# Kernel optimization log

Measured on AMD Instinct MI355X. Metric: run time of the kernel, lower is better.

The kernel has to match this reference:

```python
import jax, jax.numpy as jnp
import numpy as np

N = 100000
E = 1600000
F_IN = 128
HID = 128
C = 10
NEG_SLOPE = 0.2


def setup_inputs() -> dict:
    key = jax.random.key(0)
    ks = jax.random.split(key, 12)
    x = jax.random.normal(ks[0], (N, F_IN), dtype=jnp.float32)
    edge_index = jax.random.randint(ks[1], (2, E), 0, N, dtype=jnp.int64)
    batch = jnp.zeros((N,), dtype=jnp.int64)
    s1 = 1.0 / np.sqrt(F_IN)
    s2 = 1.0 / np.sqrt(HID)
    return {
        "x": x,
        "edge_index": edge_index,
        "batch": batch,
        "W1": jax.random.normal(ks[2], (F_IN, HID), dtype=jnp.float32) * s1,
        "a_src1": jax.random.normal(ks[3], (HID,), dtype=jnp.float32) * s2,
        "a_dst1": jax.random.normal(ks[4], (HID,), dtype=jnp.float32) * s2,
        "b1": jnp.zeros((HID,), dtype=jnp.float32),
        "W2": jax.random.normal(ks[5], (HID, HID), dtype=jnp.float32) * s2,
        "a_src2": jax.random.normal(ks[6], (HID,), dtype=jnp.float32) * s2,
        "a_dst2": jax.random.normal(ks[7], (HID,), dtype=jnp.float32) * s2,
        "b2": jnp.zeros((HID,), dtype=jnp.float32),
        "Wlin": jax.random.normal(ks[8], (HID, C), dtype=jnp.float32) * s2,
        "blin": jnp.zeros((C,), dtype=jnp.float32),
    }


def gat_conv(x, src, dst, W, a_src, a_dst, b):
    # PyG GATConv, heads=1: h = xW; alpha_e = softmax_dst(leaky_relu(a_src.h[src] + a_dst.h[dst]))
    h = x @ W                                  # [N, H]
    alpha_s = h @ a_src                        # [N]
    alpha_d = h @ a_dst                        # [N]
    e = jax.nn.leaky_relu(alpha_s[src] + alpha_d[dst], NEG_SLOPE)  # [E]
    m = jax.ops.segment_max(e, dst, num_segments=N)                # per-dst max (stable softmax)
    ex = jnp.exp(e - m[dst])
    denom = jax.ops.segment_sum(ex, dst, num_segments=N)
    alpha = ex / (denom[dst] + 1e-16)          # [E]
    out = jax.ops.segment_sum(h[src] * alpha[:, None], dst, num_segments=N)
    return out + b


def reference(x, edge_index, batch, W1, a_src1, a_dst1, b1, W2, a_src2, a_dst2, b2, Wlin, blin):
    x = x.astype(jnp.float32)
    loops = jnp.arange(N, dtype=edge_index.dtype)
    src = jnp.concatenate([edge_index[0], loops])  # add_self_loops=True
    dst = jnp.concatenate([edge_index[1], loops])
    h = jax.nn.relu(gat_conv(x, src, dst, W1, a_src1, a_dst1, b1))
    h = jax.nn.relu(gat_conv(h, src, dst, W2, a_src2, a_dst2, b2))
    # dropout(p=0.5) is identity in eval mode
    return h @ Wlin + blin
```

## Files before the change

kernel.cpp:

```cpp
#include <hip/hip_runtime.h>

#define N_NODES 100000
#define N_EDGES 1600000
#define TOTE    (N_EDGES + N_NODES)
#define NEG     0.2f
#define NB      ((N_NODES + 255) >> 8)
#define BCAP    5120

typedef __attribute__((ext_vector_type(8))) short bf16x8;
typedef __attribute__((ext_vector_type(4))) float floatx4;

__device__ __forceinline__ unsigned short f2bf(float f) {
  unsigned int u = __float_as_uint(f);
  u += 0x7fffu + ((u >> 16) & 1u);
  return (unsigned short)(u >> 16);
}
__device__ __forceinline__ float bf_lo(unsigned int r) { return __uint_as_float(r << 16); }
__device__ __forceinline__ float bf_hi(unsigned int r) { return __uint_as_float(r & 0xffff0000u); }

__global__ __launch_bounds__(256) void k_wprep(const float* __restrict__ W1, const float* __restrict__ W2,
                                               unsigned short* __restrict__ B1hi, unsigned short* __restrict__ B1lo,
                                               unsigned short* __restrict__ B2hi, unsigned short* __restrict__ B2lo,
                                               int* __restrict__ bucketCnt) {
  int b = blockIdx.x;
  int t = threadIdx.x;
  if (b == 16) {
    for (int i = t; i < NB * 16; i += 256) bucketCnt[i] = 0;
    return;
  }
  const float* W = (b < 8) ? W1 : W2;
  unsigned short* Bh = (b < 8) ? B1hi : B2hi;
  unsigned short* Bl = (b < 8) ? B1lo : B2lo;
  int ntile = b & 7;
  int kq = t >> 6, lane = t & 63;
  int q = lane >> 4, m = lane & 15;
  int n = ntile * 16 + m;
  union { unsigned short us[8]; uint4 u4; } hi, lo;
#pragma unroll
  for (int j = 0; j < 8; ++j) {
    int k = kq * 32 + q * 8 + j;
    float w = W[(size_t)k * 128 + n];
    unsigned int u = __float_as_uint(w);
    hi.us[j] = (unsigned short)(u >> 16);
    float res = w - __uint_as_float(u & 0xffff0000u);
    lo.us[j] = f2bf(res);
  }
  size_t fo = ((size_t)(ntile * 4 + kq) * 64 + lane) * 8;
  *reinterpret_cast<uint4*>(Bh + fo) = hi.u4;
  *reinterpret_cast<uint4*>(Bl + fo) = lo.u4;
}

__global__ __launch_bounds__(256) void k_binA(const int* __restrict__ ei, int* __restrict__ bucketCnt,
                                              unsigned int* __restrict__ binned) {
  __shared__ int hist[NB];
  __shared__ int cur[NB];
  int t = threadIdx.x;
  for (int b = t; b < NB; b += 256) hist[b] = 0;
  __syncthreads();
  unsigned int pk[16]; int bk[16];
#pragma unroll
  for (int j = 0; j < 16; ++j) {
    int idx = blockIdx.x * 4096 + j * 256 + t;
    if (idx < N_EDGES) {
      int s = ei[idx], d = ei[N_EDGES + idx];
      bk[j] = d >> 8;
      pk[j] = ((unsigned int)s << 8) | (unsigned int)(d & 255);
      atomicAdd(&hist[bk[j]], 1);
    } else bk[j] = -1;
  }
  __syncthreads();
  for (int b = t; b < NB; b += 256) {
    int h = hist[b];
    if (h) cur[b] = b * BCAP + atomicAdd(&bucketCnt[b * 16], h);
  }
  __syncthreads();
#pragma unroll
  for (int j = 0; j < 16; ++j) {
    if (bk[j] >= 0) {
      int pos = atomicAdd(&cur[bk[j]], 1);
      binned[pos] = pk[j];
    }
  }
}

__global__ __launch_bounds__(512) void k_bin_scan(const int* __restrict__ bucketCnt,
                                                  int* __restrict__ binOffs) {
  __shared__ int sc[512];
  int t = threadIdx.x;
  int v = (t < NB) ? bucketCnt[t * 16] : 0;
  sc[t] = v; __syncthreads();
  for (int off = 1; off < 512; off <<= 1) {
    int x = (t >= off) ? sc[t - off] : 0;
    __syncthreads();
    sc[t] += x;
    __syncthreads();
  }
  int excl = sc[t] - v;
  if (t <= NB) binOffs[t] = excl;
}

__global__ __launch_bounds__(256) void k_binB(const unsigned int* __restrict__ binned,
                                              const int* __restrict__ binOffs,
                                              int* __restrict__ offs, int* __restrict__ srcs) {
  __shared__ int cnt[256];
  __shared__ int sc[256];
  __shared__ int cur[256];
  int b = blockIdx.x;
  int t = threadIdx.x;
  int node0 = b << 8;
  int nNodes = min(256, N_NODES - node0);
  int cntE = binOffs[b + 1] - binOffs[b];
  int e0 = b * BCAP, e1 = e0 + cntE;
  int base = binOffs[b] + node0;

  cnt[t] = 0; __syncthreads();
  for (int i = e0 + t; i < e1; i += 256) atomicAdd(&cnt[binned[i] & 255u], 1);
  __syncthreads();

  int v = (t < nNodes) ? cnt[t] + 1 : 0;
  sc[t] = v; __syncthreads();
  for (int off = 1; off < 256; off <<= 1) {
    int x = (t >= off) ? sc[t - off] : 0;
    __syncthreads();
    sc[t] += x;
    __syncthreads();
  }
  int excl = sc[t] - v;
  if (t < nNodes) {
    offs[node0 + t] = base + excl;
    srcs[base + excl] = node0 + t;
  }
  cur[t] = excl + 1;
  __syncthreads();

  for (int i = e0 + t; i < e1; i += 256) {
    unsigned int e = binned[i];
    int j = (int)(e & 255u);
    int s = (int)(e >> 8);
    int p = atomicAdd(&cur[j], 1);
    srcs[base + p] = s;
  }
  if (b == 0 && t == 0) offs[N_NODES] = TOTE;
}

template <bool SPLIT>
__global__ __launch_bounds__(256) void k_gemm_mfma(const void* __restrict__ Aptr,
                                                   const unsigned short* __restrict__ Bhi,
                                                   const unsigned short* __restrict__ Blo,
                                                   unsigned short* __restrict__ Cb,
                                                   const float* __restrict__ avS, const float* __restrict__ avD,
                                                   float* __restrict__ aS, float* __restrict__ aD,
                                                   float* __restrict__ slotS, float* __restrict__ slotD) {
  __shared__ unsigned short sC[64 * 136];
  __shared__ float redS[64 * 4], redD[64 * 4];
  __shared__ float mS[64], mD[64];
  int t = threadIdx.x;
  int w = t >> 6, lane = t & 63;
  int q = lane >> 4, m = lane & 15;
  int rbase = blockIdx.x * 64;

  floatx4 acc[4][2];
#pragma unroll
  for (int mt = 0; mt < 4; ++mt)
#pragma unroll
    for (int nt = 0; nt < 2; ++nt) acc[mt][nt] = (floatx4){0.f, 0.f, 0.f, 0.f};

#pragma unroll
  for (int k0 = 0; k0 < 4; ++k0) {
    bf16x8 Bh[2], Bl[2], Ah[4], Al[4];
#pragma unroll
    for (int nt = 0; nt < 2; ++nt) {
      int ntg = w * 2 + nt;
      size_t fo = ((size_t)(ntg * 4 + k0) * 64 + lane) * 8;
      Bh[nt] = *reinterpret_cast<const bf16x8*>(Bhi + fo);
      Bl[nt] = *reinterpret_cast<const bf16x8*>(Blo + fo);
    }
#pragma unroll
    for (int mt = 0; mt < 4; ++mt) {
      int row = rbase + mt * 16 + m;
      row = min(row, N_NODES - 1);
      if constexpr (SPLIT) {
        const float* ap = (const float*)Aptr + (size_t)row * 128 + k0 * 32 + q * 8;
        float4 v0 = *reinterpret_cast<const float4*>(ap);
        float4 v1 = *reinterpret_cast<const float4*>(ap + 4);
        float av[8] = {v0.x, v0.y, v0.z, v0.w, v1.x, v1.y, v1.z, v1.w};
        union { unsigned short us[8]; bf16x8 v; } uh, ul;
#pragma unroll
        for (int j = 0; j < 8; ++j) {
          unsigned int u = __float_as_uint(av[j]);
          uh.us[j] = (unsigned short)(u >> 16);
          float res = av[j] - __uint_as_float(u & 0xffff0000u);
          ul.us[j] = f2bf(res);
        }
        Ah[mt] = uh.v; Al[mt] = ul.v;
      } else {
        const unsigned short* ap = (const unsigned short*)Aptr + (size_t)row * 128 + k0 * 32 + q * 8;
        Ah[mt] = *reinterpret_cast<const bf16x8*>(ap);
      }
    }
#pragma unroll
    for (int mt = 0; mt < 4; ++mt)
#pragma unroll
      for (int nt = 0; nt < 2; ++nt) {
        acc[mt][nt] = __builtin_amdgcn_mfma_f32_16x16x32_bf16(Ah[mt], Bh[nt], acc[mt][nt], 0, 0, 0);
        acc[mt][nt] = __builtin_amdgcn_mfma_f32_16x16x32_bf16(Ah[mt], Bl[nt], acc[mt][nt], 0, 0, 0);
        if constexpr (SPLIT)
          acc[mt][nt] = __builtin_amdgcn_mfma_f32_16x16x32_bf16(Al[mt], Bh[nt], acc[mt][nt], 0, 0, 0);
      }
  }

  float avs[2], avd[2];
#pragma unroll
  for (int nt = 0; nt < 2; ++nt) {
    int c = w * 32 + nt * 16 + m;
    avs[nt] = avS[c];
    avd[nt] = avD[c];
  }
#pragma unroll
  for (int mt = 0; mt < 4; ++mt)
#pragma unroll
    for (int r = 0; r < 4; ++r) {
      float ps = acc[mt][0][r] * avs[0] + acc[mt][1][r] * avs[1];
      float pd = acc[mt][0][r] * avd[0] + acc[mt][1][r] * avd[1];
      ps += __shfl_xor(ps, 1); pd += __shfl_xor(pd, 1);
      ps += __shfl_xor(ps, 2); pd += __shfl_xor(pd, 2);
      ps += __shfl_xor(ps, 4); pd += __shfl_xor(pd, 4);
      ps += __shfl_xor(ps, 8); pd += __shfl_xor(pd, 8);
      if (m == 0) {
        int rl = mt * 16 + q * 4 + r;
        redS[rl * 4 + w] = ps;
        redD[rl * 4 + w] = pd;
      }
    }

#pragma unroll
  for (int mt = 0; mt < 4; ++mt)
#pragma unroll
    for (int nt = 0; nt < 2; ++nt)
#pragma unroll
      for (int r = 0; r < 4; ++r) {
        int rl = mt * 16 + q * 4 + r;
        int cl = w * 32 + nt * 16 + m;
        sC[rl * 136 + cl] = f2bf(acc[mt][nt][r]);
      }
  __syncthreads();

#pragma unroll
  for (int i = 0; i < 4; ++i) {
    int idx = i * 256 + t;
    int rl = idx >> 4, kk = idx & 15;
    int gr = rbase + rl;
    if (gr < N_NODES)
      *reinterpret_cast<uint4*>(Cb + (size_t)gr * 128 + kk * 8) =
          *reinterpret_cast<const uint4*>(sC + rl * 136 + kk * 8);
  }

  if (t < 64) {
    int gr = rbase + t;
    bool ok = gr < N_NODES;
    float ps = redS[t * 4] + redS[t * 4 + 1] + redS[t * 4 + 2] + redS[t * 4 + 3];
    float pd = redD[t * 4] + redD[t * 4 + 1] + redD[t * 4 + 2] + redD[t * 4 + 3];
    if (ok) { aS[gr] = ps; aD[gr] = pd; }
    mS[t] = ok ? ps : -1e30f;
    mD[t] = ok ? pd : -1e30f;
  }
  __syncthreads();
#pragma unroll
  for (int off = 32; off > 0; off >>= 1) {
    if (t < off) { mS[t] = fmaxf(mS[t], mS[t + off]); mD[t] = fmaxf(mD[t], mD[t + off]); }
    __syncthreads();
  }
  if (t == 0) { slotS[blockIdx.x] = mS[0]; slotD[blockIdx.x] = mD[0]; }
}

__global__ __launch_bounds__(256) void k_gmax(const float* __restrict__ slotS,
                                              const float* __restrict__ slotD,
                                              int n, float* __restrict__ gMh) {
  __shared__ float sS[256], sD[256];
  int t = threadIdx.x;
  float ms = -1e30f, md = -1e30f;
  for (int i = t; i < n; i += 256) { ms = fmaxf(ms, slotS[i]); md = fmaxf(md, slotD[i]); }
  sS[t] = ms; sD[t] = md;
  __syncthreads();
#pragma unroll
  for (int off = 128; off > 0; off >>= 1) {
    if (t < off) { sS[t] = fmaxf(sS[t], sS[t + off]); sD[t] = fmaxf(sD[t], sD[t + off]); }
    __syncthreads();
  }
  if (t == 0) {
    float M = sS[0] + sD[0];
    gMh[0] = (M > 0.f) ? M : NEG * M;
  }
}

#define FMA8(E, R)                                     \
  do {                                                 \
    acc[0] += (E) * bf_lo((R).x); acc[1] += (E) * bf_hi((R).x); \
    acc[2] += (E) * bf_lo((R).y); acc[3] += (E) * bf_hi((R).y); \
    acc[4] += (E) * bf_lo((R).z); acc[5] += (E) * bf_hi((R).z); \
    acc[6] += (E) * bf_lo((R).w); acc[7] += (E) * bf_hi((R).w); \
  } while (0)

#define LDG(R0, R1, R2, R3, E0, E1, E2, E3, J)                                                   \
  do {                                                                                           \
    float2 q0 = pairs[pbase + (J) + 0];                                                          \
    float2 q1 = pairs[pbase + (J) + 1];                                                          \
    float2 q2 = pairs[pbase + (J) + 2];                                                          \
    float2 q3 = pairs[pbase + (J) + 3];                                                          \
    E0 = q0.x; E1 = q1.x; E2 = q2.x; E3 = q3.x;                                                  \
    R0 = *reinterpret_cast<const uint4*>(hbl + ((size_t)(unsigned)__float_as_int(q0.y) << 7));   \
    R1 = *reinterpret_cast<const uint4*>(hbl + ((size_t)(unsigned)__float_as_int(q1.y) << 7));   \
    R2 = *reinterpret_cast<const uint4*>(hbl + ((size_t)(unsigned)__float_as_int(q2.y) << 7));   \
    R3 = *reinterpret_cast<const uint4*>(hbl + ((size_t)(unsigned)__float_as_int(q3.y) << 7));   \
  } while (0)
#define FMAG(R0, R1, R2, R3, E0, E1, E2, E3) \
  do { FMA8(E0, R0); FMA8(E1, R1); FMA8(E2, R2); FMA8(E3, R3); } while (0)

template <bool FINAL>
__global__ __launch_bounds__(256) void k_aggregate(const unsigned short* __restrict__ hb,
                                                   const float* __restrict__ aS,
                                                   const float* __restrict__ aD,
                                                   const int* __restrict__ offs,
                                                   const int* __restrict__ srcs,
                                                   const float* __restrict__ bias,
                                                   const float* __restrict__ gMh,
                                                   unsigned short* __restrict__ outb,
                                                   const float* __restrict__ Wl,
                                                   const float* __restrict__ bl,
                                                   float* __restrict__ out) {
  __shared__ float2 pairs[16 * 17];
  __shared__ float sWt[FINAL ? 10 * 144 : 1];
  __shared__ float sbl[FINAL ? 16 : 1];
  int t = threadIdx.x;
  if constexpr (FINAL) {
    if (t < 128) {
      int jj = t >> 5, ii = t & 31;
#pragma unroll
      for (int c = 0; c < 10; ++c) sWt[c * 144 + jj * 36 + ii] = Wl[t * 10 + c];
    }
    if (t < 10) sbl[t] = bl[t];
    __syncthreads();
  }
  int g = t >> 4;
  int l = t & 15;
  int dst = blockIdx.x * 16 + g;
  float Mh = gMh[0];
  int beg = offs[dst], end = offs[dst + 1];
  float adn = aD[dst];
  float denom = 0.f;
  float acc[8];
#pragma unroll
  for (int k = 0; k < 8; ++k) acc[k] = 0.f;
  const int pbase = g * 17;
  const unsigned short* hbl = hb + l * 8;

  uint4 ra0, ra1, ra2, ra3, rb0, rb1, rb2, rb3;
  float ea0, ea1, ea2, ea3, eb0, eb1, eb2, eb3;

  for (int chunk = beg; chunk < end; chunk += 16) {
    int i = chunk + l;
    float ex = 0.f; int s = 0;
    if (i < end) {
      s = srcs[i];
      float e = aS[s] + adn;
      e = (e > 0.f) ? e : NEG * e;
      ex = __expf(e - Mh);
    }
    denom += ex;
    pairs[pbase + l] = make_float2(ex, __int_as_float(s));
    int cnt = end - chunk; if (cnt > 16) cnt = 16;
    LDG(ra0, ra1, ra2, ra3, ea0, ea1, ea2, ea3, 0);
    int j = 0;
    for (;;) {
      bool more = (j + 4) < cnt;
      if (more) LDG(rb0, rb1, rb2, rb3, eb0, eb1, eb2, eb3, j + 4);
      FMAG(ra0, ra1, ra2, ra3, ea0, ea1, ea2, ea3);
      j += 4;
      if (!more) break;
      bool more2 = (j + 4) < cnt;
      if (more2) LDG(ra0, ra1, ra2, ra3, ea0, ea1, ea2, ea3, j + 4);
      FMAG(rb0, rb1, rb2, rb3, eb0, eb1, eb2, eb3);
      j += 4;
      if (!more2) break;
    }
  }

  denom += __shfl_xor(denom, 1);
  denom += __shfl_xor(denom, 2);
  denom += __shfl_xor(denom, 4);
  denom += __shfl_xor(denom, 8);
  float inv = 1.f / (denom + 1e-16f);
  float4 b0 = *reinterpret_cast<const float4*>(bias + l * 8);
  float4 b1 = *reinterpret_cast<const float4*>(bias + l * 8 + 4);
  float o0 = fmaxf(acc[0] * inv + b0.x, 0.f), o1 = fmaxf(acc[1] * inv + b0.y, 0.f);
  float o2 = fmaxf(acc[2] * inv + b0.z, 0.f), o3 = fmaxf(acc[3] * inv + b0.w, 0.f);
  float o4 = fmaxf(acc[4] * inv + b1.x, 0.f), o5 = fmaxf(acc[5] * inv + b1.y, 0.f);
  float o6 = fmaxf(acc[6] * inv + b1.z, 0.f), o7 = fmaxf(acc[7] * inv + b1.w, 0.f);

  if constexpr (!FINAL) {
    union { unsigned short us[8]; uint4 u4; } oo;
    oo.us[0] = f2bf(o0); oo.us[1] = f2bf(o1); oo.us[2] = f2bf(o2); oo.us[3] = f2bf(o3);
    oo.us[4] = f2bf(o4); oo.us[5] = f2bf(o5); oo.us[6] = f2bf(o6); oo.us[7] = f2bf(o7);
    *reinterpret_cast<uint4*>(outb + (size_t)dst * 128 + l * 8) = oo.u4;
  } else {
    float p[10];
#pragma unroll
    for (int c = 0; c < 10; ++c) {
      const float4* wp = reinterpret_cast<const float4*>(&sWt[c * 144 + (l >> 2) * 36 + (l & 3) * 8]);
      float4 w0 = wp[0], w1 = wp[1];
      p[c] = o0 * w0.x + o1 * w0.y + o2 * w0.z + o3 * w0.w +
             o4 * w1.x + o5 * w1.y + o6 * w1.z + o7 * w1.w;
    }
#pragma unroll
    for (int c = 0; c < 10; ++c) {
      p[c] += __shfl_xor(p[c], 1);
      p[c] += __shfl_xor(p[c], 2);
      p[c] += __shfl_xor(p[c], 4);
      p[c] += __shfl_xor(p[c], 8);
    }
    if (l == 0) {
      float* orow = out + (size_t)dst * 10;
      *reinterpret_cast<float2*>(orow + 0) = make_float2(p[0] + sbl[0], p[1] + sbl[1]);
      *reinterpret_cast<float2*>(orow + 2) = make_float2(p[2] + sbl[2], p[3] + sbl[3]);
      *reinterpret_cast<float2*>(orow + 4) = make_float2(p[4] + sbl[4], p[5] + sbl[5]);
      *reinterpret_cast<float2*>(orow + 6) = make_float2(p[6] + sbl[6], p[7] + sbl[7]);
      *reinterpret_cast<float2*>(orow + 8) = make_float2(p[8] + sbl[8], p[9] + sbl[9]);
    }
  }
}

extern "C" void kernel_launch(void* const* d_in, const int* in_sizes, int n_in,
                              void* d_out, int out_size, void* d_ws, size_t ws_size,
                              hipStream_t stream) {
  const float* x   = (const float*)d_in[0];
  const int*   ei  = (const int*)d_in[1];
  const float* W1  = (const float*)d_in[3];
  const float* as1 = (const float*)d_in[4];
  const float* ad1 = (const float*)d_in[5];
  const float* b1  = (const float*)d_in[6];
  const float* W2  = (const float*)d_in[7];
  const float* as2 = (const float*)d_in[8];
  const float* ad2 = (const float*)d_in[9];
  const float* b2  = (const float*)d_in[10];
  const float* Wl  = (const float*)d_in[11];
  const float* bl  = (const float*)d_in[12];
  float* out = (float*)d_out;

  char* p = (char*)d_ws;
  unsigned short* hb   = (unsigned short*)p; p += (size_t)N_NODES * 128 * sizeof(unsigned short);
  unsigned short* hagg = (unsigned short*)p; p += (size_t)N_NODES * 128 * sizeof(unsigned short);
  float* aS    = (float*)p; p += (size_t)N_NODES * sizeof(float);
  float* aD    = (float*)p; p += (size_t)N_NODES * sizeof(float);
  int* offs    = (int*)p;   p += (size_t)(N_NODES + 4) * sizeof(int);
  int* srcs    = (int*)p;   p += (size_t)TOTE * sizeof(int);
  int* bucketCnt = (int*)p; p += (size_t)NB * 16 * sizeof(int);
  int* binOffs   = (int*)p; p += (size_t)(NB + 4) * sizeof(int);
  float* slotS = (float*)p; p += 2048 * sizeof(float);
  float* slotD = (float*)p; p += 2048 * sizeof(float);
  float* gMh = (float*)p;   p += 4 * sizeof(float);
  unsigned short* B1hi = (unsigned short*)p; p += 128 * 128 * sizeof(unsigned short);
  unsigned short* B1lo = (unsigned short*)p; p += 128 * 128 * sizeof(unsigned short);
  unsigned short* B2hi = (unsigned short*)p; p += 128 * 128 * sizeof(unsigned short);
  unsigned short* B2lo = (unsigned short*)p; p += 128 * 128 * sizeof(unsigned short);
  unsigned int* binned = (unsigned int*)hagg;

  int binBlocks = (N_EDGES + 4095) / 4096;

  k_wprep<<<17, 256, 0, stream>>>(W1, W2, B1hi, B1lo, B2hi, B2lo, bucketCnt);
  k_binA<<<binBlocks, 256, 0, stream>>>(ei, bucketCnt, binned);
  k_bin_scan<<<1, 512, 0, stream>>>(bucketCnt, binOffs);
  k_binB<<<NB, 256, 0, stream>>>(binned, binOffs, offs, srcs);

  int gemmBlocks = (N_NODES + 63) / 64;
  int aggBlocks  = N_NODES / 16;

  k_gemm_mfma<true><<<gemmBlocks, 256, 0, stream>>>(x, B1hi, B1lo, hb, as1, ad1, aS, aD, slotS, slotD);
  k_gmax<<<1, 256, 0, stream>>>(slotS, slotD, gemmBlocks, gMh);
  k_aggregate<false><<<aggBlocks, 256, 0, stream>>>(hb, aS, aD, offs, srcs, b1, gMh, hagg,
                                                    nullptr, nullptr, nullptr);
  k_gemm_mfma<false><<<gemmBlocks, 256, 0, stream>>>(hagg, B2hi, B2lo, hb, as2, ad2, aS, aD, slotS, slotD);
  k_gmax<<<1, 256, 0, stream>>>(slotS, slotD, gemmBlocks, gMh);
  k_aggregate<true><<<aggBlocks, 256, 0, stream>>>(hb, aS, aD, offs, srcs, b2, gMh, hagg,
                                                   Wl, bl, out);
}
```

Baseline: 353.1 us.

## Precompute per-edge softmax weights and denominators in separate edge-prep kernel

Edge attention weights (exp of leaky-relu scores) and per-destination denominators are moved out of the aggregation kernel into a new edge-prep kernel that writes (weight, src) pairs to a global array. The CSR source list now packs the local destination index into its low bits so edge-prep can work per 256-node bucket with shared-memory atomics. The aggregation kernel then streams the precomputed pairs straight from global memory, with no shared-memory staging or shuffle reduction, and prefetches them one group ahead. This adds an extra kernel launch and about 13.6 MB of pair traffic per layer in exchange for a simpler, more latency-tolerant gather loop.

Result: slower. 397.5 us (+12.6%).

```diff
diff --git a/kernel.cpp b/kernel.cpp
--- a/kernel.cpp
+++ b/kernel.cpp
@@ -101,7 +101,7 @@
 
 __global__ __launch_bounds__(256) void k_binB(const unsigned int* __restrict__ binned,
                                               const int* __restrict__ binOffs,
-                                              int* __restrict__ offs, int* __restrict__ srcs) {
+                                              int* __restrict__ offs, unsigned int* __restrict__ srcs) {
   __shared__ int cnt[256];
   __shared__ int sc[256];
   __shared__ int cur[256];
@@ -128,7 +128,7 @@
   int excl = sc[t] - v;
   if (t < nNodes) {
     offs[node0 + t] = base + excl;
-    srcs[base + excl] = node0 + t;
+    srcs[base + excl] = ((unsigned int)(node0 + t) << 8) | (unsigned int)t;
   }
   cur[t] = excl + 1;
   __syncthreads();
@@ -136,9 +136,8 @@
   for (int i = e0 + t; i < e1; i += 256) {
     unsigned int e = binned[i];
     int j = (int)(e & 255u);
-    int s = (int)(e >> 8);
     int p = atomicAdd(&cur[j], 1);
-    srcs[base + p] = s;
+    srcs[base + p] = e;
   }
   if (b == 0 && t == 0) offs[N_NODES] = TOTE;
 }
@@ -293,6 +292,37 @@
   }
 }
 
+__global__ __launch_bounds__(256) void k_edgeprep(const unsigned int* __restrict__ srcs,
+                                                  const int* __restrict__ binOffs,
+                                                  const float* __restrict__ aS,
+                                                  const float* __restrict__ aD,
+                                                  const float* __restrict__ gMh,
+                                                  float2* __restrict__ pairEx,
+                                                  float* __restrict__ denomG) {
+  __shared__ float sden[256];
+  int b = blockIdx.x;
+  int t = threadIdx.x;
+  int node0 = b << 8;
+  int nNodes = min(256, N_NODES - node0);
+  int e0 = binOffs[b] + node0;
+  int e1 = binOffs[b + 1] + node0 + nNodes;
+  float Mh = gMh[0];
+  sden[t] = 0.f;
+  __syncthreads();
+  for (int i = e0 + t; i < e1; i += 256) {
+    unsigned int pk = srcs[i];
+    int j = (int)(pk & 255u);
+    int s = (int)(pk >> 8);
+    float e = aS[s] + aD[node0 + j];
+    e = (e > 0.f) ? e : NEG * e;
+    float ex = __expf(e - Mh);
+    pairEx[i] = make_float2(ex, __int_as_float(s));
+    atomicAdd(&sden[j], ex);
+  }
+  __syncthreads();
+  if (t < nNodes) denomG[node0 + t] = sden[t];
+}
+
 #define FMA8(E, R)                                     \
   do {                                                 \
     acc[0] += (E) * bf_lo((R).x); acc[1] += (E) * bf_hi((R).x); \
@@ -301,34 +331,35 @@
     acc[6] += (E) * bf_lo((R).w); acc[7] += (E) * bf_hi((R).w); \
   } while (0)
 
-#define LDG(R0, R1, R2, R3, E0, E1, E2, E3, J)                                                   \
-  do {                                                                                           \
-    float2 q0 = pairs[pbase + (J) + 0];                                                          \
-    float2 q1 = pairs[pbase + (J) + 1];                                                          \
-    float2 q2 = pairs[pbase + (J) + 2];                                                          \
-    float2 q3 = pairs[pbase + (J) + 3];                                                          \
-    E0 = q0.x; E1 = q1.x; E2 = q2.x; E3 = q3.x;                                                  \
-    R0 = *reinterpret_cast<const uint4*>(hbl + ((size_t)(unsigned)__float_as_int(q0.y) << 7));   \
-    R1 = *reinterpret_cast<const uint4*>(hbl + ((size_t)(unsigned)__float_as_int(q1.y) << 7));   \
-    R2 = *reinterpret_cast<const uint4*>(hbl + ((size_t)(unsigned)__float_as_int(q2.y) << 7));   \
-    R3 = *reinterpret_cast<const uint4*>(hbl + ((size_t)(unsigned)__float_as_int(q3.y) << 7));   \
+#define LOADP(Q0, Q1, Q2, Q3, J)                               \
+  do {                                                         \
+    Q0 = ((J) + 0 < n) ? pp[(J) + 0] : zf2;                    \
+    Q1 = ((J) + 1 < n) ? pp[(J) + 1] : zf2;                    \
+    Q2 = ((J) + 2 < n) ? pp[(J) + 2] : zf2;                    \
+    Q3 = ((J) + 3 < n) ? pp[(J) + 3] : zf2;                    \
   } while (0)
-#define FMAG(R0, R1, R2, R3, E0, E1, E2, E3) \
-  do { FMA8(E0, R0); FMA8(E1, R1); FMA8(E2, R2); FMA8(E3, R3); } while (0)
+
+#define GATH(R0, R1, R2, R3, Q0, Q1, Q2, Q3)                                                       \
+  do {                                                                                             \
+    R0 = *reinterpret_cast<const uint4*>(hbl + ((size_t)(unsigned)__float_as_int((Q0).y) << 7));   \
+    R1 = *reinterpret_cast<const uint4*>(hbl + ((size_t)(unsigned)__float_as_int((Q1).y) << 7));   \
+    R2 = *reinterpret_cast<const uint4*>(hbl + ((size_t)(unsigned)__float_as_int((Q2).y) << 7));   \
+    R3 = *reinterpret_cast<const uint4*>(hbl + ((size_t)(unsigned)__float_as_int((Q3).y) << 7));   \
+  } while (0)
+
+#define FMAG(R0, R1, R2, R3, Q0, Q1, Q2, Q3) \
+  do { FMA8((Q0).x, R0); FMA8((Q1).x, R1); FMA8((Q2).x, R2); FMA8((Q3).x, R3); } while (0)
 
 template <bool FINAL>
 __global__ __launch_bounds__(256) void k_aggregate(const unsigned short* __restrict__ hb,
-                                                   const float* __restrict__ aS,
-                                                   const float* __restrict__ aD,
+                                                   const float2* __restrict__ pairEx,
                                                    const int* __restrict__ offs,
-                                                   const int* __restrict__ srcs,
+                                                   const float* __restrict__ denomG,
                                                    const float* __restrict__ bias,
-                                                   const float* __restrict__ gMh,
                                                    unsigned short* __restrict__ outb,
                                                    const float* __restrict__ Wl,
                                                    const float* __restrict__ bl,
                                                    float* __restrict__ out) {
-  __shared__ float2 pairs[16 * 17];
   __shared__ float sWt[FINAL ? 10 * 144 : 1];
   __shared__ float sbl[FINAL ? 16 : 1];
   int t = threadIdx.x;
@@ -344,52 +375,39 @@
   int g = t >> 4;
   int l = t & 15;
   int dst = blockIdx.x * 16 + g;
-  float Mh = gMh[0];
   int beg = offs[dst], end = offs[dst + 1];
-  float adn = aD[dst];
-  float denom = 0.f;
+  int n = end - beg;
+  float den = denomG[dst];
   float acc[8];
 #pragma unroll
   for (int k = 0; k < 8; ++k) acc[k] = 0.f;
-  const int pbase = g * 17;
+  const float2* pp = pairEx + beg;
   const unsigned short* hbl = hb + l * 8;
-
+  const float2 zf2 = make_float2(0.f, 0.f);
+
+  float2 qa0, qa1, qa2, qa3, qb0, qb1, qb2, qb3;
   uint4 ra0, ra1, ra2, ra3, rb0, rb1, rb2, rb3;
-  float ea0, ea1, ea2, ea3, eb0, eb1, eb2, eb3;
-
-  for (int chunk = beg; chunk < end; chunk += 16) {
-    int i = chunk + l;
-    float ex = 0.f; int s = 0;
-    if (i < end) {
-      s = srcs[i];
-      float e = aS[s] + adn;
-      e = (e > 0.f) ? e : NEG * e;
-      ex = __expf(e - Mh);
-    }
-    denom += ex;
-    pairs[pbase + l] = make_float2(ex, __int_as_float(s));
-    int cnt = end - chunk; if (cnt > 16) cnt = 16;
-    LDG(ra0, ra1, ra2, ra3, ea0, ea1, ea2, ea3, 0);
-    int j = 0;
-    for (;;) {
-      bool more = (j + 4) < cnt;
-      if (more) LDG(rb0, rb1, rb2, rb3, eb0, eb1, eb2, eb3, j + 4);
-      FMAG(ra0, ra1, ra2, ra3, ea0, ea1, ea2, ea3);
-      j += 4;
-      if (!more) break;
-      bool more2 = (j + 4) < cnt;
-      if (more2) LDG(ra0, ra1, ra2, ra3, ea0, ea1, ea2, ea3, j + 4);
-      FMAG(rb0, rb1, rb2, rb3, eb0, eb1, eb2, eb3);
-      j += 4;
-      if (!more2) break;
-    }
-  }
-
-  denom += __shfl_xor(denom, 1);
-  denom += __shfl_xor(denom, 2);
-  denom += __shfl_xor(denom, 4);
-  denom += __shfl_xor(denom, 8);
-  float inv = 1.f / (denom + 1e-16f);
+
+  LOADP(qa0, qa1, qa2, qa3, 0);
+  if (4 < n) LOADP(qb0, qb1, qb2, qb3, 4);
+  GATH(ra0, ra1, ra2, ra3, qa0, qa1, qa2, qa3);
+  int j = 0;
+  for (;;) {
+    bool m1 = (j + 4) < n;
+    if (m1) GATH(rb0, rb1, rb2, rb3, qb0, qb1, qb2, qb3);
+    FMAG(ra0, ra1, ra2, ra3, qa0, qa1, qa2, qa3);
+    if ((j + 8) < n) LOADP(qa0, qa1, qa2, qa3, j + 8);
+    j += 4;
+    if (!m1) break;
+    bool m2 = (j + 4) < n;
+    if (m2) GATH(ra0, ra1, ra2, ra3, qa0, qa1, qa2, qa3);
+    FMAG(rb0, rb1, rb2, rb3, qb0, qb1, qb2, qb3);
+    if ((j + 8) < n) LOADP(qb0, qb1, qb2, qb3, j + 8);
+    j += 4;
+    if (!m2) break;
+  }
+
+  float inv = 1.f / (den + 1e-16f);
   float4 b0 = *reinterpret_cast<const float4*>(bias + l * 8);
   float4 b1 = *reinterpret_cast<const float4*>(bias + l * 8 + 4);
   float o0 = fmaxf(acc[0] * inv + b0.x, 0.f), o1 = fmaxf(acc[1] * inv + b0.y, 0.f);
@@ -452,7 +470,7 @@
   float* aS    = (float*)p; p += (size_t)N_NODES * sizeof(float);
   float* aD    = (float*)p; p += (size_t)N_NODES * sizeof(float);
   int* offs    = (int*)p;   p += (size_t)(N_NODES + 4) * sizeof(int);
-  int* srcs    = (int*)p;   p += (size_t)TOTE * sizeof(int);
+  unsigned int* srcs = (unsigned int*)p; p += (size_t)TOTE * sizeof(unsigned int);
   int* bucketCnt = (int*)p; p += (size_t)NB * 16 * sizeof(int);
   int* binOffs   = (int*)p; p += (size_t)(NB + 4) * sizeof(int);
   float* slotS = (float*)p; p += 2048 * sizeof(float);
@@ -462,6 +480,8 @@
   unsigned short* B1lo = (unsigned short*)p; p += 128 * 128 * sizeof(unsigned short);
   unsigned short* B2hi = (unsigned short*)p; p += 128 * 128 * sizeof(unsigned short);
   unsigned short* B2lo = (unsigned short*)p; p += 128 * 128 * sizeof(unsigned short);
+  float* denomG = (float*)p; p += (size_t)N_NODES * sizeof(float);
+  float2* pairEx = (float2*)p; p += (size_t)TOTE * sizeof(float2);
   unsigned int* binned = (unsigned int*)hagg;
 
   int binBlocks = (N_EDGES + 4095) / 4096;
@@ -476,10 +496,12 @@
 
   k_gemm_mfma<true><<<gemmBlocks, 256, 0, stream>>>(x, B1hi, B1lo, hb, as1, ad1, aS, aD, slotS, slotD);
   k_gmax<<<1, 256, 0, stream>>>(slotS, slotD, gemmBlocks, gMh);
-  k_aggregate<false><<<aggBlocks, 256, 0, stream>>>(hb, aS, aD, offs, srcs, b1, gMh, hagg,
+  k_edgeprep<<<NB, 256, 0, stream>>>(srcs, binOffs, aS, aD, gMh, pairEx, denomG);
+  k_aggregate<false><<<aggBlocks, 256, 0, stream>>>(hb, pairEx, offs, denomG, b1, hagg,
                                                     nullptr, nullptr, nullptr);
   k_gemm_mfma<false><<<gemmBlocks, 256, 0, stream>>>(hagg, B2hi, B2lo, hb, as2, ad2, aS, aD, slotS, slotD);
   k_gmax<<<1, 256, 0, stream>>>(slotS, slotD, gemmBlocks, gMh);
-  k_aggregate<true><<<aggBlocks, 256, 0, stream>>>(hb, aS, aD, offs, srcs, b2, gMh, hagg,
+  k_edgeprep<<<NB, 256, 0, stream>>>(srcs, binOffs, aS, aD, gMh, pairEx, denomG);
+  k_aggregate<true><<<aggBlocks, 256, 0, stream>>>(hb, pairEx, offs, denomG, b2, hagg,
                                                    Wl, bl, out);
 }
```

## Remove scan and gmax kernels via atomics, shrink aggregate blocks, simplify gather loop

Applied to the files above, without the earlier changes.

Three small kernels are removed. The bucket prefix scan is folded into each binB block as a redundant block-level reduction over preceding buckets. The per-block max slots plus the separate k_gmax kernel are replaced by an order-preserving float encoding with global atomicMax, zeroed in k_wprep. The aggregate kernel moves from 256 to 128 threads per block (8 destinations per block), and its double-buffered software-pipelined gather is replaced by a plain unrolled loop of four loads with a scalar tail. This saves launch and serialization overhead, but binB now does O(NB) redundant reads per block and the gather may expose more load latency.

Result: slower. 403.8 us (+14.4%).

```diff
diff --git a/kernel.cpp b/kernel.cpp
--- a/kernel.cpp
+++ b/kernel.cpp
@@ -18,14 +18,24 @@
 __device__ __forceinline__ float bf_lo(unsigned int r) { return __uint_as_float(r << 16); }
 __device__ __forceinline__ float bf_hi(unsigned int r) { return __uint_as_float(r & 0xffff0000u); }
 
+__device__ __forceinline__ unsigned int fenc(float f) {
+  unsigned int u = __float_as_uint(f);
+  return (u & 0x80000000u) ? ~u : (u | 0x80000000u);
+}
+__device__ __forceinline__ float fdec(unsigned int c) {
+  unsigned int u = (c & 0x80000000u) ? (c & 0x7fffffffu) : ~c;
+  return __uint_as_float(u);
+}
+
 __global__ __launch_bounds__(256) void k_wprep(const float* __restrict__ W1, const float* __restrict__ W2,
                                                unsigned short* __restrict__ B1hi, unsigned short* __restrict__ B1lo,
                                                unsigned short* __restrict__ B2hi, unsigned short* __restrict__ B2lo,
-                                               int* __restrict__ bucketCnt) {
+                                               int* __restrict__ bucketCnt, unsigned int* __restrict__ gmx) {
   int b = blockIdx.x;
   int t = threadIdx.x;
   if (b == 16) {
     for (int i = t; i < NB * 16; i += 256) bucketCnt[i] = 0;
+    if (t < 4) gmx[t] = 0u;
     return;
   }
   const float* W = (b < 8) ? W1 : W2;
@@ -83,25 +93,10 @@
   }
 }
 
-__global__ __launch_bounds__(512) void k_bin_scan(const int* __restrict__ bucketCnt,
-                                                  int* __restrict__ binOffs) {
-  __shared__ int sc[512];
-  int t = threadIdx.x;
-  int v = (t < NB) ? bucketCnt[t * 16] : 0;
-  sc[t] = v; __syncthreads();
-  for (int off = 1; off < 512; off <<= 1) {
-    int x = (t >= off) ? sc[t - off] : 0;
-    __syncthreads();
-    sc[t] += x;
-    __syncthreads();
-  }
-  int excl = sc[t] - v;
-  if (t <= NB) binOffs[t] = excl;
-}
-
 __global__ __launch_bounds__(256) void k_binB(const unsigned int* __restrict__ binned,
-                                              const int* __restrict__ binOffs,
+                                              const int* __restrict__ bucketCnt,
                                               int* __restrict__ offs, int* __restrict__ srcs) {
+  __shared__ int red[256];
   __shared__ int cnt[256];
   __shared__ int sc[256];
   __shared__ int cur[256];
@@ -109,9 +104,19 @@
   int t = threadIdx.x;
   int node0 = b << 8;
   int nNodes = min(256, N_NODES - node0);
-  int cntE = binOffs[b + 1] - binOffs[b];
+
+  int a = 0;
+  for (int i = t; i < b; i += 256) a += bucketCnt[i * 16];
+  red[t] = a; __syncthreads();
+#pragma unroll
+  for (int off = 128; off > 0; off >>= 1) {
+    if (t < off) red[t] += red[t + off];
+    __syncthreads();
+  }
+  int pre = red[0];
+  int cntE = bucketCnt[b * 16];
   int e0 = b * BCAP, e1 = e0 + cntE;
-  int base = binOffs[b] + node0;
+  int base = pre + node0;
 
   cnt[t] = 0; __syncthreads();
   for (int i = e0 + t; i < e1; i += 256) atomicAdd(&cnt[binned[i] & 255u], 1);
@@ -150,7 +155,7 @@
                                                    unsigned short* __restrict__ Cb,
                                                    const float* __restrict__ avS, const float* __restrict__ avD,
                                                    float* __restrict__ aS, float* __restrict__ aD,
-                                                   float* __restrict__ slotS, float* __restrict__ slotD) {
+                                                   unsigned int* __restrict__ gmx) {
   __shared__ unsigned short sC[64 * 136];
   __shared__ float redS[64 * 4], redD[64 * 4];
   __shared__ float mS[64], mD[64];
@@ -270,26 +275,9 @@
     if (t < off) { mS[t] = fmaxf(mS[t], mS[t + off]); mD[t] = fmaxf(mD[t], mD[t + off]); }
     __syncthreads();
   }
-  if (t == 0) { slotS[blockIdx.x] = mS[0]; slotD[blockIdx.x] = mD[0]; }
-}
-
-__global__ __launch_bounds__(256) void k_gmax(const float* __restrict__ slotS,
-                                              const float* __restrict__ slotD,
-                                              int n, float* __restrict__ gMh) {
-  __shared__ float sS[256], sD[256];
-  int t = threadIdx.x;
-  float ms = -1e30f, md = -1e30f;
-  for (int i = t; i < n; i += 256) { ms = fmaxf(ms, slotS[i]); md = fmaxf(md, slotD[i]); }
-  sS[t] = ms; sD[t] = md;
-  __syncthreads();
-#pragma unroll
-  for (int off = 128; off > 0; off >>= 1) {
-    if (t < off) { sS[t] = fmaxf(sS[t], sS[t + off]); sD[t] = fmaxf(sD[t], sD[t + off]); }
-    __syncthreads();
-  }
   if (t == 0) {
-    float M = sS[0] + sD[0];
-    gMh[0] = (M > 0.f) ? M : NEG * M;
+    atomicMax(&gmx[0], fenc(mS[0]));
+    atomicMax(&gmx[1], fenc(mD[0]));
   }
 }
 
@@ -301,39 +289,24 @@
     acc[6] += (E) * bf_lo((R).w); acc[7] += (E) * bf_hi((R).w); \
   } while (0)
 
-#define LDG(R0, R1, R2, R3, E0, E1, E2, E3, J)                                                   \
-  do {                                                                                           \
-    float2 q0 = pairs[pbase + (J) + 0];                                                          \
-    float2 q1 = pairs[pbase + (J) + 1];                                                          \
-    float2 q2 = pairs[pbase + (J) + 2];                                                          \
-    float2 q3 = pairs[pbase + (J) + 3];                                                          \
-    E0 = q0.x; E1 = q1.x; E2 = q2.x; E3 = q3.x;                                                  \
-    R0 = *reinterpret_cast<const uint4*>(hbl + ((size_t)(unsigned)__float_as_int(q0.y) << 7));   \
-    R1 = *reinterpret_cast<const uint4*>(hbl + ((size_t)(unsigned)__float_as_int(q1.y) << 7));   \
-    R2 = *reinterpret_cast<const uint4*>(hbl + ((size_t)(unsigned)__float_as_int(q2.y) << 7));   \
-    R3 = *reinterpret_cast<const uint4*>(hbl + ((size_t)(unsigned)__float_as_int(q3.y) << 7));   \
-  } while (0)
-#define FMAG(R0, R1, R2, R3, E0, E1, E2, E3) \
-  do { FMA8(E0, R0); FMA8(E1, R1); FMA8(E2, R2); FMA8(E3, R3); } while (0)
-
 template <bool FINAL>
-__global__ __launch_bounds__(256) void k_aggregate(const unsigned short* __restrict__ hb,
+__global__ __launch_bounds__(128) void k_aggregate(const unsigned short* __restrict__ hb,
                                                    const float* __restrict__ aS,
                                                    const float* __restrict__ aD,
                                                    const int* __restrict__ offs,
                                                    const int* __restrict__ srcs,
                                                    const float* __restrict__ bias,
-                                                   const float* __restrict__ gMh,
+                                                   const unsigned int* __restrict__ gmx,
                                                    unsigned short* __restrict__ outb,
                                                    const float* __restrict__ Wl,
                                                    const float* __restrict__ bl,
                                                    float* __restrict__ out) {
-  __shared__ float2 pairs[16 * 17];
+  __shared__ float2 pairs[8 * 17];
   __shared__ float sWt[FINAL ? 10 * 144 : 1];
   __shared__ float sbl[FINAL ? 16 : 1];
   int t = threadIdx.x;
   if constexpr (FINAL) {
-    if (t < 128) {
+    {
       int jj = t >> 5, ii = t & 31;
 #pragma unroll
       for (int c = 0; c < 10; ++c) sWt[c * 144 + jj * 36 + ii] = Wl[t * 10 + c];
@@ -343,8 +316,9 @@
   }
   int g = t >> 4;
   int l = t & 15;
-  int dst = blockIdx.x * 16 + g;
-  float Mh = gMh[0];
+  int dst = blockIdx.x * 8 + g;
+  float M = fdec(gmx[0]) + fdec(gmx[1]);
+  float Mh = (M > 0.f) ? M : NEG * M;
   int beg = offs[dst], end = offs[dst + 1];
   float adn = aD[dst];
   float denom = 0.f;
@@ -352,10 +326,6 @@
 #pragma unroll
   for (int k = 0; k < 8; ++k) acc[k] = 0.f;
   const int pbase = g * 17;
-  const unsigned short* hbl = hb + l * 8;
-
-  uint4 ra0, ra1, ra2, ra3, rb0, rb1, rb2, rb3;
-  float ea0, ea1, ea2, ea3, eb0, eb1, eb2, eb3;
 
   for (int chunk = beg; chunk < end; chunk += 16) {
     int i = chunk + l;
@@ -368,23 +338,28 @@
     }
     denom += ex;
     pairs[pbase + l] = make_float2(ex, __int_as_float(s));
-    int cnt = end - chunk; if (cnt > 16) cnt = 16;
-    LDG(ra0, ra1, ra2, ra3, ea0, ea1, ea2, ea3, 0);
+    int cnt = min(16, end - chunk);
     int j = 0;
-    for (;;) {
-      bool more = (j + 4) < cnt;
-      if (more) LDG(rb0, rb1, rb2, rb3, eb0, eb1, eb2, eb3, j + 4);
-      FMAG(ra0, ra1, ra2, ra3, ea0, ea1, ea2, ea3);
-      j += 4;
-      if (!more) break;
-      bool more2 = (j + 4) < cnt;
-      if (more2) LDG(ra0, ra1, ra2, ra3, ea0, ea1, ea2, ea3, j + 4);
-      FMAG(rb0, rb1, rb2, rb3, eb0, eb1, eb2, eb3);
-      j += 4;
-      if (!more2) break;
-    }
-  }
-
+    for (; j + 4 <= cnt; j += 4) {
+      float2 p0 = pairs[pbase + j + 0];
+      float2 p1 = pairs[pbase + j + 1];
+      float2 p2 = pairs[pbase + j + 2];
+      float2 p3 = pairs[pbase + j + 3];
+      uint4 r0 = *reinterpret_cast<const uint4*>(hb + (size_t)__float_as_int(p0.y) * 128 + l * 8);
+      uint4 r1 = *reinterpret_cast<const uint4*>(hb + (size_t)__float_as_int(p1.y) * 128 + l * 8);
+      uint4 r2 = *reinterpret_cast<const uint4*>(hb + (size_t)__float_as_int(p2.y) * 128 + l * 8);
+      uint4 r3 = *reinterpret_cast<const uint4*>(hb + (size_t)__float_as_int(p3.y) * 128 + l * 8);
+      FMA8(p0.x, r0);
+      FMA8(p1.x, r1);
+      FMA8(p2.x, r2);
+      FMA8(p3.x, r3);
+    }
+    for (; j < cnt; ++j) {
+      float2 pp = pairs[pbase + j];
+      uint4 r = *reinterpret_cast<const uint4*>(hb + (size_t)__float_as_int(pp.y) * 128 + l * 8);
+      FMA8(pp.x, r);
+    }
+  }
   denom += __shfl_xor(denom, 1);
   denom += __shfl_xor(denom, 2);
   denom += __shfl_xor(denom, 4);
@@ -454,10 +429,7 @@
   int* offs    = (int*)p;   p += (size_t)(N_NODES + 4) * sizeof(int);
   int* srcs    = (int*)p;   p += (size_t)TOTE * sizeof(int);
   int* bucketCnt = (int*)p; p += (size_t)NB * 16 * sizeof(int);
-  int* binOffs   = (int*)p; p += (size_t)(NB + 4) * sizeof(int);
-  float* slotS = (float*)p; p += 2048 * sizeof(float);
-  float* slotD = (float*)p; p += 2048 * sizeof(float);
-  float* gMh = (float*)p;   p += 4 * sizeof(float);
+  unsigned int* gmx = (unsigned int*)p; p += 16 * sizeof(unsigned int);
   unsigned short* B1hi = (unsigned short*)p; p += 128 * 128 * sizeof(unsigned short);
   unsigned short* B1lo = (unsigned short*)p; p += 128 * 128 * sizeof(unsigned short);
   unsigned short* B2hi = (unsigned short*)p; p += 128 * 128 * sizeof(unsigned short);
@@ -466,20 +438,17 @@
 
   int binBlocks = (N_EDGES + 4095) / 4096;
 
-  k_wprep<<<17, 256, 0, stream>>>(W1, W2, B1hi, B1lo, B2hi, B2lo, bucketCnt);
+  k_wprep<<<17, 256, 0, stream>>>(W1, W2, B1hi, B1lo, B2hi, B2lo, bucketCnt, gmx);
   k_binA<<<binBlocks, 256, 0, stream>>>(ei, bucketCnt, binned);
-  k_bin_scan<<<1, 512, 0, stream>>>(bucketCnt, binOffs);
-  k_binB<<<NB, 256, 0, stream>>>(binned, binOffs, offs, srcs);
+  k_binB<<<NB, 256, 0, stream>>>(binned, bucketCnt, offs, srcs);
 
   int gemmBlocks = (N_NODES + 63) / 64;
-  int aggBlocks  = N_NODES / 16;
-
-  k_gemm_mfma<true><<<gemmBlocks, 256, 0, stream>>>(x, B1hi, B1lo, hb, as1, ad1, aS, aD, slotS, slotD);
-  k_gmax<<<1, 256, 0, stream>>>(slotS, slotD, gemmBlocks, gMh);
-  k_aggregate<false><<<aggBlocks, 256, 0, stream>>>(hb, aS, aD, offs, srcs, b1, gMh, hagg,
+  int aggBlocks  = N_NODES / 8;
+
+  k_gemm_mfma<true><<<gemmBlocks, 256, 0, stream>>>(x, B1hi, B1lo, hb, as1, ad1, aS, aD, gmx);
+  k_aggregate<false><<<aggBlocks, 128, 0, stream>>>(hb, aS, aD, offs, srcs, b1, gmx, hagg,
                                                     nullptr, nullptr, nullptr);
-  k_gemm_mfma<false><<<gemmBlocks, 256, 0, stream>>>(hagg, B2hi, B2lo, hb, as2, ad2, aS, aD, slotS, slotD);
-  k_gmax<<<1, 256, 0, stream>>>(slotS, slotD, gemmBlocks, gMh);
-  k_aggregate<true><<<aggBlocks, 256, 0, stream>>>(hb, aS, aD, offs, srcs, b2, gMh, hagg,
+  k_gemm_mfma<false><<<gemmBlocks, 256, 0, stream>>>(hagg, B2hi, B2lo, hb, as2, ad2, aS, aD, gmx + 2);
+  k_aggregate<true><<<aggBlocks, 128, 0, stream>>>(hb, aS, aD, offs, srcs, b2, gmx + 2, hagg,
                                                    Wl, bl, out);
 }
```

## Stage GEMM A tiles into LDS via async global_load_lds; simplify aggregate loop

Applied to the files above, without the earlier changes.

The GEMM kernel now loads its 64-row A tile into a padded LDS buffer with global_load_lds direct-to-LDS transfers before the MFMA loop, reads A fragments from LDS, and reuses that buffer for the output staging. This replaces strided per-lane global reads with coalesced bulk loads, and adds an occupancy hint of 4 blocks per CU. The aggregate kernel drops the manual double-buffered software prefetch in favour of a simple unroll-by-4 loop with a scalar tail, handing load scheduling to the compiler. The simpler loop may hide gather latency less well, and the larger LDS buffer (about 33KB in the split case) may limit occupancy.

New measurement: 347.6 us. About the same (-1.6%).

```diff
diff --git a/kernel.cpp b/kernel.cpp
--- a/kernel.cpp
+++ b/kernel.cpp
@@ -144,26 +144,44 @@
 }
 
 template <bool SPLIT>
-__global__ __launch_bounds__(256) void k_gemm_mfma(const void* __restrict__ Aptr,
+__global__ __launch_bounds__(256, 4) void k_gemm_mfma(const void* __restrict__ Aptr,
                                                    const unsigned short* __restrict__ Bhi,
                                                    const unsigned short* __restrict__ Blo,
                                                    unsigned short* __restrict__ Cb,
                                                    const float* __restrict__ avS, const float* __restrict__ avD,
                                                    float* __restrict__ aS, float* __restrict__ aD,
                                                    float* __restrict__ slotS, float* __restrict__ slotD) {
-  __shared__ unsigned short sC[64 * 136];
+  constexpr int SRCB  = SPLIT ? 512 : 256;
+  constexpr int ROWB  = SPLIT ? 528 : 272;
+  constexpr int ABYTES = 64 * ROWB;
+  constexpr int CHUNKS = ABYTES / 1024;
+  __shared__ char sbuf[ABYTES];
   __shared__ float redS[64 * 4], redD[64 * 4];
   __shared__ float mS[64], mD[64];
   int t = threadIdx.x;
   int w = t >> 6, lane = t & 63;
   int q = lane >> 4, m = lane & 15;
   int rbase = blockIdx.x * 64;
+  const char* Ab = (const char*)Aptr;
+
+  for (int c = w; c < CHUNKS; c += 4) {
+    int L = c * 1024 + lane * 16;
+    int r = L / ROWB;
+    int off = L - r * ROWB;
+    int gr = min(rbase + r, N_NODES - 1);
+    const char* src = (off < SRCB) ? (Ab + (size_t)gr * SRCB + off) : Ab;
+    __builtin_amdgcn_global_load_lds((const __attribute__((address_space(1))) void*)src,
+                                     (__attribute__((address_space(3))) void*)(sbuf + c * 1024),
+                                     16, 0, 0);
+  }
 
   floatx4 acc[4][2];
 #pragma unroll
   for (int mt = 0; mt < 4; ++mt)
 #pragma unroll
     for (int nt = 0; nt < 2; ++nt) acc[mt][nt] = (floatx4){0.f, 0.f, 0.f, 0.f};
+
+  __syncthreads();
 
 #pragma unroll
   for (int k0 = 0; k0 < 4; ++k0) {
@@ -177,12 +195,11 @@
     }
 #pragma unroll
     for (int mt = 0; mt < 4; ++mt) {
-      int row = rbase + mt * 16 + m;
-      row = min(row, N_NODES - 1);
+      int R = mt * 16 + m;
       if constexpr (SPLIT) {
-        const float* ap = (const float*)Aptr + (size_t)row * 128 + k0 * 32 + q * 8;
+        const char* ap = sbuf + R * ROWB + k0 * 128 + q * 32;
         float4 v0 = *reinterpret_cast<const float4*>(ap);
-        float4 v1 = *reinterpret_cast<const float4*>(ap + 4);
+        float4 v1 = *reinterpret_cast<const float4*>(ap + 16);
         float av[8] = {v0.x, v0.y, v0.z, v0.w, v1.x, v1.y, v1.z, v1.w};
         union { unsigned short us[8]; bf16x8 v; } uh, ul;
 #pragma unroll
@@ -194,8 +211,7 @@
         }
         Ah[mt] = uh.v; Al[mt] = ul.v;
       } else {
-        const unsigned short* ap = (const unsigned short*)Aptr + (size_t)row * 128 + k0 * 32 + q * 8;
-        Ah[mt] = *reinterpret_cast<const bf16x8*>(ap);
+        Ah[mt] = *reinterpret_cast<const bf16x8*>(sbuf + R * ROWB + k0 * 64 + q * 16);
       }
     }
 #pragma unroll
@@ -233,6 +249,9 @@
       }
     }
 
+  __syncthreads();
+  unsigned short* sC = (unsigned short*)sbuf;
+
 #pragma unroll
   for (int mt = 0; mt < 4; ++mt)
 #pragma unroll
@@ -300,21 +319,6 @@
     acc[4] += (E) * bf_lo((R).z); acc[5] += (E) * bf_hi((R).z); \
     acc[6] += (E) * bf_lo((R).w); acc[7] += (E) * bf_hi((R).w); \
   } while (0)
-
-#define LDG(R0, R1, R2, R3, E0, E1, E2, E3, J)                                                   \
-  do {                                                                                           \
-    float2 q0 = pairs[pbase + (J) + 0];                                                          \
-    float2 q1 = pairs[pbase + (J) + 1];                                                          \
-    float2 q2 = pairs[pbase + (J) + 2];                                                          \
-    float2 q3 = pairs[pbase + (J) + 3];                                                          \
-    E0 = q0.x; E1 = q1.x; E2 = q2.x; E3 = q3.x;                                                  \
-    R0 = *reinterpret_cast<const uint4*>(hbl + ((size_t)(unsigned)__float_as_int(q0.y) << 7));   \
-    R1 = *reinterpret_cast<const uint4*>(hbl + ((size_t)(unsigned)__float_as_int(q1.y) << 7));   \
-    R2 = *reinterpret_cast<const uint4*>(hbl + ((size_t)(unsigned)__float_as_int(q2.y) << 7));   \
-    R3 = *reinterpret_cast<const uint4*>(hbl + ((size_t)(unsigned)__float_as_int(q3.y) << 7));   \
-  } while (0)
-#define FMAG(R0, R1, R2, R3, E0, E1, E2, E3) \
-  do { FMA8(E0, R0); FMA8(E1, R1); FMA8(E2, R2); FMA8(E3, R3); } while (0)
 
 template <bool FINAL>
 __global__ __launch_bounds__(256) void k_aggregate(const unsigned short* __restrict__ hb,
@@ -352,10 +356,6 @@
 #pragma unroll
   for (int k = 0; k < 8; ++k) acc[k] = 0.f;
   const int pbase = g * 17;
-  const unsigned short* hbl = hb + l * 8;
-
-  uint4 ra0, ra1, ra2, ra3, rb0, rb1, rb2, rb3;
-  float ea0, ea1, ea2, ea3, eb0, eb1, eb2, eb3;
 
   for (int chunk = beg; chunk < end; chunk += 16) {
     int i = chunk + l;
@@ -368,23 +368,28 @@
     }
     denom += ex;
     pairs[pbase + l] = make_float2(ex, __int_as_float(s));
-    int cnt = end - chunk; if (cnt > 16) cnt = 16;
-    LDG(ra0, ra1, ra2, ra3, ea0, ea1, ea2, ea3, 0);
+    int cnt = min(16, end - chunk);
     int j = 0;
-    for (;;) {
-      bool more = (j + 4) < cnt;
-      if (more) LDG(rb0, rb1, rb2, rb3, eb0, eb1, eb2, eb3, j + 4);
-      FMAG(ra0, ra1, ra2, ra3, ea0, ea1, ea2, ea3);
-      j += 4;
-      if (!more) break;
-      bool more2 = (j + 4) < cnt;
-      if (more2) LDG(ra0, ra1, ra2, ra3, ea0, ea1, ea2, ea3, j + 4);
-      FMAG(rb0, rb1, rb2, rb3, eb0, eb1, eb2, eb3);
-      j += 4;
-      if (!more2) break;
-    }
-  }
-
+    for (; j + 4 <= cnt; j += 4) {
+      float2 p0 = pairs[pbase + j + 0];
+      float2 p1 = pairs[pbase + j + 1];
+      float2 p2 = pairs[pbase + j + 2];
+      float2 p3 = pairs[pbase + j + 3];
+      uint4 r0 = *reinterpret_cast<const uint4*>(hb + (size_t)__float_as_int(p0.y) * 128 + l * 8);
+      uint4 r1 = *reinterpret_cast<const uint4*>(hb + (size_t)__float_as_int(p1.y) * 128 + l * 8);
+      uint4 r2 = *reinterpret_cast<const uint4*>(hb + (size_t)__float_as_int(p2.y) * 128 + l * 8);
+      uint4 r3 = *reinterpret_cast<const uint4*>(hb + (size_t)__float_as_int(p3.y) * 128 + l * 8);
+      FMA8(p0.x, r0);
+      FMA8(p1.x, r1);
+      FMA8(p2.x, r2);
+      FMA8(p3.x, r3);
+    }
+    for (; j < cnt; ++j) {
+      float2 pp = pairs[pbase + j];
+      uint4 r = *reinterpret_cast<const uint4*>(hb + (size_t)__float_as_int(pp.y) * 128 + l * 8);
+      FMA8(pp.x, r);
+    }
+  }
   denom += __shfl_xor(denom, 1);
   denom += __shfl_xor(denom, 2);
   denom += __shfl_xor(denom, 4);
```
